# Kernel tuning notes

Hardware: AMD Instinct MI355X
Metric: run time of the kernel (lower is better)

The kernel has to match this reference:

```python
import jax, jax.numpy as jnp
import numpy as np
import math

B, L, D = 2, 2048, 1024
H = 16
DH = D // H  # 64
XPOS_SCALE_BASE = 512.0
THETA = 10000.0


def setup_inputs() -> dict:
    key = jax.random.key(0)
    ks = jax.random.split(key, 9)
    s = 0.02  # keep logits in a sane range like trained weights
    return {
        "x": jax.random.normal(ks[0], (B, L, D), dtype=jnp.float32),
        "Wq": jax.random.normal(ks[1], (D, D), dtype=jnp.float32) * s,
        "bq": jax.random.normal(ks[2], (D,), dtype=jnp.float32) * s,
        "Wk": jax.random.normal(ks[3], (D, D), dtype=jnp.float32) * s,
        "bk": jax.random.normal(ks[4], (D,), dtype=jnp.float32) * s,
        "Wv": jax.random.normal(ks[5], (D, D), dtype=jnp.float32) * s,
        "bv": jax.random.normal(ks[6], (D,), dtype=jnp.float32) * s,
        "Wo": jax.random.normal(ks[7], (D, D), dtype=jnp.float32) * s,
        "bo": jax.random.normal(ks[8], (D,), dtype=jnp.float32) * s,
    }


def _rotate_half(t):
    # pairwise interleaved rotation, as in rotary_embedding_torch
    t1 = t[..., 0::2]
    t2 = t[..., 1::2]
    return jnp.stack([-t2, t1], axis=-1).reshape(t.shape)


def _xpos_rotate(q, k):
    # q, k: [B, H, L, DH]; xPos rotary embedding (use_xpos=True)
    seq = q.shape[2]
    half = jnp.arange(0, DH, 2, dtype=jnp.float32)
    inv_freq = 1.0 / (THETA ** (half / DH))            # [DH/2]
    t = jnp.arange(seq, dtype=jnp.float32)             # [L]
    freqs = t[:, None] * inv_freq[None, :]             # [L, DH/2]
    freqs = jnp.repeat(freqs, 2, axis=-1)              # [L, DH] interleaved
    # xPos length-extrapolatable scale
    scale_vec = (half + 0.4 * DH) / (1.4 * DH)         # [DH/2]
    power = (t - seq // 2) / XPOS_SCALE_BASE           # [L]
    scale = scale_vec[None, :] ** power[:, None]       # [L, DH/2]
    scale = jnp.repeat(scale, 2, axis=-1)              # [L, DH]
    cos = jnp.cos(freqs)
    sin = jnp.sin(freqs)
    q_out = q * (cos * scale) + _rotate_half(q) * (sin * scale)
    k_out = k * (cos / scale) + _rotate_half(k) * (sin / scale)
    return q_out, k_out


def reference(x, Wq, bq, Wk, bk, Wv, bv, Wo, bo):
    b, l, d = x.shape
    # projections; note source swaps names: v_mat <- k-proj, k_mat <- v-proj
    q = (x @ Wq.T + bq).reshape(b, l, H, DH).transpose(0, 2, 1, 3)  # [b,h,l,dh]
    v = (x @ Wk.T + bk).reshape(b, l, H, DH).transpose(0, 2, 1, 3)
    k = (x @ Wv.T + bv).reshape(b, l, H, DH).transpose(0, 2, 1, 3)
    q, k = _xpos_rotate(q, k)
    # source divides by sqrt(Dh * num_heads) == sqrt(dim)
    scores = jnp.einsum("bhqd,bhkd->bhqk", q, k) / math.sqrt(d)
    weights = jax.nn.softmax(scores, axis=-1)
    inter = jnp.einsum("bhqk,bhkd->bhqd", weights, v)
    inter = inter.transpose(0, 2, 1, 3).reshape(b, l, d)
    return inter @ Wo.T + bo
```

## Files before the change

kernel.cpp:

```cpp
#include <hip/hip_runtime.h>
#include <math.h>

#define NB 2
#define NL 2048
#define ND 1024
#define NH 16
#define NDH 64
#define NBL 4096

typedef __attribute__((ext_vector_type(4)))  float f32x4;
typedef __attribute__((ext_vector_type(16))) float f32x16;
typedef __attribute__((ext_vector_type(8)))  short s16x8;
typedef __attribute__((ext_vector_type(4)))  short s16x4;

#define LOG2E 1.44269504088896f

__device__ __forceinline__ float fexp2(float x){
#if __has_builtin(__builtin_amdgcn_exp2f)
  return __builtin_amdgcn_exp2f(x);
#else
  return exp2f(x);
#endif
}

__device__ __forceinline__ unsigned short f2bf(float f){
  unsigned int u = __float_as_uint(f);
  u += 0x7FFF + ((u >> 16) & 1);
  return (unsigned short)(u >> 16);
}

__device__ __forceinline__ unsigned int pk2bf(float lo, float hi){
  return __builtin_amdgcn_perm(__float_as_uint(hi) + 0x8000u,
                               __float_as_uint(lo) + 0x8000u, 0x07060302u);
}

__global__ void cvt_all(const float* __restrict__ x,
                        const float* __restrict__ wq, const float* __restrict__ wk,
                        const float* __restrict__ wv, const float* __restrict__ wo,
                        unsigned short* __restrict__ xb,
                        unsigned short* __restrict__ wqb, unsigned short* __restrict__ wkb,
                        unsigned short* __restrict__ wvb, unsigned short* __restrict__ wob){
  int i = blockIdx.x * blockDim.x + threadIdx.x;
  const float* s; unsigned short* d; int off;
  if (i < (1<<20)) { s = x; d = xb; off = i; }
  else {
    int j = i - (1<<20); int w = j >> 18; off = j & ((1<<18)-1);
    s = (w==0)?wq:(w==1)?wk:(w==2)?wv:wo;
    d = (w==0)?wqb:(w==1)?wkb:(w==2)?wvb:wob;
  }
  float4 f = reinterpret_cast<const float4*>(s)[off];
  ushort4 r; r.x=f2bf(f.x); r.y=f2bf(f.y); r.z=f2bf(f.z); r.w=f2bf(f.w);
  reinterpret_cast<ushort4*>(d)[off] = r;
}

__global__ void rope_tables(float2* __restrict__ qtab, float2* __restrict__ ktab){
  int t = blockIdx.x * blockDim.x + threadIdx.x;
  int l = t >> 5, i = t & 31;
  float half = 2.0f * (float)i;
  float inv_freq = 1.0f / powf(10000.0f, half / 64.0f);
  float fr = (float)l * inv_freq;
  float sv = (half + 0.4f * 64.0f) / (1.4f * 64.0f);
  float pw = ((float)l - 1024.0f) / 512.0f;
  float sc = powf(sv, pw);
  float cs = cosf(fr), sn = sinf(fr);
  qtab[t] = make_float2(cs * sc, sn * sc);
  ktab[t] = make_float2(cs / sc, sn / sc);
}

__device__ __forceinline__ void gemm_core128(
    const unsigned short* __restrict__ A, const unsigned short* __restrict__ W,
    int row0, int col0,
    unsigned short (&As)[128][32], unsigned short (&Bs)[128][32],
    f32x4 (&acc)[4][4])
{
  const int tid  = threadIdx.x;
  const int wave = tid >> 6, lane = tid & 63;
  const int m16  = lane & 15, quad = lane >> 4;
  const int mrow = (wave & 1) * 64, ncol = (wave >> 1) * 64;
  const int rA   = lane >> 2, cA = (lane & 3) * 8;

  for (int k0 = 0; k0 < ND; k0 += 32){
    __syncthreads();
#pragma unroll
    for (int i2 = 0; i2 < 2; i2++){
      const int c = wave * 2 + i2;
      const unsigned short* ga = A + (size_t)(row0 + c*16 + rA) * ND + k0 + cA;
      const unsigned short* gb = W + (size_t)(col0 + c*16 + rA) * ND + k0 + cA;
      __builtin_amdgcn_global_load_lds((const __attribute__((address_space(1))) void*)ga,
                                       (__attribute__((address_space(3))) void*)&As[c*16][0], 16, 0, 0);
      __builtin_amdgcn_global_load_lds((const __attribute__((address_space(1))) void*)gb,
                                       (__attribute__((address_space(3))) void*)&Bs[c*16][0], 16, 0, 0);
    }
    __syncthreads();
    s16x8 af[4], bf[4];
#pragma unroll
    for (int mt = 0; mt < 4; mt++) af[mt] = *reinterpret_cast<const s16x8*>(&As[mrow + mt*16 + m16][quad*8]);
#pragma unroll
    for (int nt = 0; nt < 4; nt++) bf[nt] = *reinterpret_cast<const s16x8*>(&Bs[ncol + nt*16 + m16][quad*8]);
#pragma unroll
    for (int mt = 0; mt < 4; mt++)
#pragma unroll
      for (int nt = 0; nt < 4; nt++)
        acc[mt][nt] = __builtin_amdgcn_mfma_f32_16x16x32_bf16(af[mt], bf[nt], acc[mt][nt], 0, 0, 0);
  }
}

__global__ __launch_bounds__(256) void gemm_qkv(
    const unsigned short* __restrict__ A,
    const unsigned short* __restrict__ Wq, const float* __restrict__ bq,
    const unsigned short* __restrict__ Wk, const float* __restrict__ bk,
    const unsigned short* __restrict__ Wv, const float* __restrict__ bv,
    unsigned short* __restrict__ qb, unsigned short* __restrict__ kb,
    unsigned short* __restrict__ vtb,
    const float2* __restrict__ qtab, const float2* __restrict__ ktab)
{
  __shared__ unsigned short As[128][32];
  __shared__ unsigned short Bs[128][32];
  __shared__ unsigned short T[128][72];

  const int mode = blockIdx.z;
  const unsigned short* W = (mode==0) ? Wq : (mode==1) ? Wk : Wv;
  const float* bias       = (mode==0) ? bq : (mode==1) ? bk : bv;

  const int row0 = blockIdx.x * 128, col0 = blockIdx.y * 128;
  f32x4 acc[4][4] = {};
  gemm_core128(A, W, row0, col0, As, Bs, acc);

  const int tid  = threadIdx.x;
  const int wave = tid >> 6, lane = tid & 63;
  const int m16  = lane & 15, quad = lane >> 4;
  const int mrow = (wave & 1) * 64, ncol = (wave >> 1) * 64;

  if (mode == 2){
    const int b = row0 >> 11, l0 = row0 & (NL - 1);
#pragma unroll
    for (int h2 = 0; h2 < 2; h2++){
      __syncthreads();
      if ((wave >> 1) == h2){
#pragma unroll
        for (int mt = 0; mt < 4; mt++)
#pragma unroll
          for (int nt = 0; nt < 4; nt++)
#pragma unroll
            for (int r = 0; r < 4; r++){
              int lrow = mrow + mt*16 + quad*4 + r;
              int dh   = nt*16 + m16;
              T[lrow][dh] = f2bf(acc[mt][nt][r] + bias[col0 + h2*64 + dh]);
            }
      }
      __syncthreads();
      const int bh = b * NH + (col0 >> 6) + h2;
#pragma unroll
      for (int j4 = 0; j4 < 4; j4++){
        int c = tid * 4 + j4;
        int d = c >> 4, seg = (c & 15) * 8;
        unsigned short tmp[8];
#pragma unroll
        for (int jj = 0; jj < 8; jj++) tmp[jj] = T[seg + jj][d];
        *reinterpret_cast<uint4*>(vtb + (size_t)(bh * NDH + d) * NL + l0 + seg) =
            *reinterpret_cast<uint4*>(tmp);
      }
    }
  } else {
    const float qscale = (mode == 0) ? (0.03125f * LOG2E) : 1.0f;
    const float2* tab  = (mode == 0) ? qtab : ktab;
    unsigned short* dst = (mode == 0) ? qb : kb;
#pragma unroll
    for (int mt = 0; mt < 4; mt++)
#pragma unroll
      for (int nt = 0; nt < 4; nt++)
#pragma unroll
        for (int r = 0; r < 4; r++){
          int grow = row0 + mrow + mt*16 + quad*4 + r;
          int gcol = col0 + ncol + nt*16 + m16;
          float v = acc[mt][nt][r] + bias[gcol];
          int b = grow >> 11, l = grow & (NL - 1);
          int h = gcol >> 6, dh = gcol & 63;
          float pv = __shfl_xor(v, 1);
          float2 t = tab[l*32 + (dh >> 1)];
          float rh = (dh & 1) ? pv : -pv;
          float ov = (v * t.x + rh * t.y) * qscale;
          dst[(((size_t)(b * NH + h)) * NL + l) * NDH + dh] = f2bf(ov);
        }
  }
}

__global__ __launch_bounds__(256) void gemm_o(
    const unsigned short* __restrict__ A, const unsigned short* __restrict__ W,
    const float* __restrict__ bias, float* __restrict__ out)
{
  __shared__ unsigned short As[128][32];
  __shared__ unsigned short Bs[64][32];
  const int tid  = threadIdx.x;
  const int wave = tid >> 6, lane = tid & 63;
  const int m16  = lane & 15, quad = lane >> 4;
  const int mrow = (wave & 1) * 64, ncol = (wave >> 1) * 32;
  const int rA   = lane >> 2, cA = (lane & 3) * 8;
  const int row0 = blockIdx.x * 128, col0 = blockIdx.y * 64;

  f32x4 acc[4][2] = {};

  for (int k0 = 0; k0 < ND; k0 += 32){
    __syncthreads();
#pragma unroll
    for (int i3 = 0; i3 < 3; i3++){
      const int c = wave * 3 + i3;
      const unsigned short* g; unsigned short* l;
      if (c < 8){ g = A + (size_t)(row0 + c*16 + rA) * ND + k0 + cA;      l = &As[c*16][0]; }
      else      { g = W + (size_t)(col0 + (c-8)*16 + rA) * ND + k0 + cA;  l = &Bs[(c-8)*16][0]; }
      __builtin_amdgcn_global_load_lds((const __attribute__((address_space(1))) void*)g,
                                       (__attribute__((address_space(3))) void*)l, 16, 0, 0);
    }
    __syncthreads();
    s16x8 af[4], bf[2];
#pragma unroll
    for (int mt = 0; mt < 4; mt++) af[mt] = *reinterpret_cast<const s16x8*>(&As[mrow + mt*16 + m16][quad*8]);
#pragma unroll
    for (int nt = 0; nt < 2; nt++) bf[nt] = *reinterpret_cast<const s16x8*>(&Bs[ncol + nt*16 + m16][quad*8]);
#pragma unroll
    for (int mt = 0; mt < 4; mt++)
#pragma unroll
      for (int nt = 0; nt < 2; nt++)
        acc[mt][nt] = __builtin_amdgcn_mfma_f32_16x16x32_bf16(af[mt], bf[nt], acc[mt][nt], 0, 0, 0);
  }

#pragma unroll
  for (int mt = 0; mt < 4; mt++)
#pragma unroll
    for (int nt = 0; nt < 2; nt++)
#pragma unroll
      for (int r = 0; r < 4; r++){
        int grow = row0 + mrow + mt*16 + quad*4 + r;
        int gcol = col0 + ncol + nt*16 + m16;
        out[(size_t)grow * ND + gcol] = acc[mt][nt][r] + bias[gcol];
      }
}

__global__ __launch_bounds__(256, 1) void attn_kernel(
    const unsigned short* __restrict__ qb,
    const unsigned short* __restrict__ kb,
    const unsigned short* __restrict__ vtb,
    unsigned short* __restrict__ ob)
{
  __shared__ unsigned short smem[256 * 72];
  const int tid  = threadIdx.x;
  const int wave = tid >> 6, lane = tid & 63;
  const int l31  = lane & 31, g = lane >> 5;
  const int bh   = blockIdx.y;
  const int q0   = blockIdx.x * 256;
  const unsigned short* Q  = qb  + (size_t)bh * NL * NDH;
  const unsigned short* K  = kb  + (size_t)bh * NL * NDH;
  const unsigned short* Vt = vtb + (size_t)bh * NDH * NL;

  s16x8 qf[2][4];
#pragma unroll
  for (int q2 = 0; q2 < 2; q2++)
#pragma unroll
    for (int s = 0; s < 4; s++)
      qf[q2][s] = *reinterpret_cast<const s16x8*>(
          Q + (size_t)(q0 + wave*64 + q2*32 + l31) * NDH + s*16 + g*8);

  const int r0 = tid >> 3,          c0 = tid & 7;
  const int r1 = (tid + 256) >> 3,  c1 = tid & 7;
  const int so0 = r0*64 + ((c0 ^ (r0 & 7)) * 8);
  const int so1 = r1*64 + ((c1 ^ (r1 & 7)) * 8);

  uint4 kreg0 = *reinterpret_cast<const uint4*>(K  + (size_t)r0 * NDH + c0*8);
  uint4 kreg1 = *reinterpret_cast<const uint4*>(K  + (size_t)r1 * NDH + c1*8);
  uint4 vreg0 = *reinterpret_cast<const uint4*>(Vt + (size_t)r0 * NL  + c0*8);
  uint4 vreg1 = *reinterpret_cast<const uint4*>(Vt + (size_t)r1 * NL  + c1*8);
  *reinterpret_cast<uint4*>(&smem[so0])         = kreg0;
  *reinterpret_cast<uint4*>(&smem[so1])         = kreg1;
  *reinterpret_cast<uint4*>(&smem[8192 + so0])  = vreg0;
  *reinterpret_cast<uint4*>(&smem[8192 + so1])  = vreg1;
  kreg0 = *reinterpret_cast<const uint4*>(K  + (size_t)(64 + r0) * NDH + c0*8);
  kreg1 = *reinterpret_cast<const uint4*>(K  + (size_t)(64 + r1) * NDH + c1*8);
  vreg0 = *reinterpret_cast<const uint4*>(Vt + (size_t)r0 * NL + 64 + c0*8);
  vreg1 = *reinterpret_cast<const uint4*>(Vt + (size_t)r1 * NL + 64 + c1*8);
  __syncthreads();

  float ls[2] = {0.f, 0.f};
  f32x16 ot[2][2] = {};
  const int key7 = l31 & 7;

  for (int kt = 0; kt < 32; kt++){
    const int cur = (kt & 1) * 4096;
    const int nxt = 4096 - cur;
    if (kt < 31){
      *reinterpret_cast<uint4*>(&smem[nxt + so0])        = kreg0;
      *reinterpret_cast<uint4*>(&smem[nxt + so1])        = kreg1;
      *reinterpret_cast<uint4*>(&smem[8192 + nxt + so0]) = vreg0;
      *reinterpret_cast<uint4*>(&smem[8192 + nxt + so1]) = vreg1;
    }
    if (kt < 30){
      const int k0n = (kt + 2) * 64;
      kreg0 = *reinterpret_cast<const uint4*>(K  + (size_t)(k0n + r0) * NDH + c0*8);
      kreg1 = *reinterpret_cast<const uint4*>(K  + (size_t)(k0n + r1) * NDH + c1*8);
      vreg0 = *reinterpret_cast<const uint4*>(Vt + (size_t)r0 * NL + k0n + c0*8);
      vreg1 = *reinterpret_cast<const uint4*>(Vt + (size_t)r1 * NL + k0n + c1*8);
    }

    const unsigned short* Kb = &smem[cur];
    const unsigned short* Vb = &smem[8192 + cur];

    unsigned int pe[2][2][8];
#pragma unroll
    for (int t = 0; t < 2; t++){
      f32x16 st0 = {}, st1 = {};
#pragma unroll
      for (int s = 0; s < 4; s++){
        const int cg = (2*s + g) ^ key7;
        s16x8 kf = *reinterpret_cast<const s16x8*>(&Kb[(t*32 + l31)*64 + cg*8]);
        st0 = __builtin_amdgcn_mfma_f32_32x32x16_bf16(kf, qf[0][s], st0, 0, 0, 0);
        st1 = __builtin_amdgcn_mfma_f32_32x32x16_bf16(kf, qf[1][s], st1, 0, 0, 0);
      }
#pragma unroll
      for (int i = 0; i < 8; i++){
        float a0 = fexp2(st0[2*i]), a1 = fexp2(st0[2*i+1]);
        ls[0] += a0 + a1;
        pe[0][t][i] = pk2bf(a0, a1);
        float b0 = fexp2(st1[2*i]), b1 = fexp2(st1[2*i+1]);
        ls[1] += b0 + b1;
        pe[1][t][i] = pk2bf(b0, b1);
      }
    }

#pragma unroll
    for (int mt = 0; mt < 2; mt++){
      const int dh = mt*32 + l31;
#pragma unroll
      for (int s = 0; s < 8; s++){
        const int cg = s ^ (dh & 7);
        s16x4 vf = *reinterpret_cast<const s16x4*>(&Vb[dh*64 + cg*8 + g*4]);
        uint2 pb0; pb0.x = pe[0][s>>2][2*(s&3)]; pb0.y = pe[0][s>>2][2*(s&3)+1];
        ot[mt][0] = __builtin_amdgcn_mfma_f32_32x32x8bf16_1k(
            vf, *reinterpret_cast<s16x4*>(&pb0), ot[mt][0], 0, 0, 0);
        uint2 pb1; pb1.x = pe[1][s>>2][2*(s&3)]; pb1.y = pe[1][s>>2][2*(s&3)+1];
        ot[mt][1] = __builtin_amdgcn_mfma_f32_32x32x8bf16_1k(
            vf, *reinterpret_cast<s16x4*>(&pb1), ot[mt][1], 0, 0, 0);
      }
    }
    __syncthreads();
  }

  float linv[2];
#pragma unroll
  for (int q2 = 0; q2 < 2; q2++){
    float t = ls[q2] + __shfl_xor(ls[q2], 32);
    linv[q2] = 1.0f / t;
  }

#pragma unroll
  for (int mt = 0; mt < 2; mt++)
#pragma unroll
    for (int q2 = 0; q2 < 2; q2++)
#pragma unroll
      for (int s = 0; s < 4; s++){
        float o0 = ot[mt][q2][4*s    ] * linv[q2];
        float o1 = ot[mt][q2][4*s + 1] * linv[q2];
        float o2 = ot[mt][q2][4*s + 2] * linv[q2];
        float o3 = ot[mt][q2][4*s + 3] * linv[q2];
        uint2 pk; pk.x = pk2bf(o0, o1); pk.y = pk2bf(o2, o3);
        *reinterpret_cast<uint2*>(&smem[(wave*64 + q2*32 + l31)*72 + mt*32 + s*8 + g*4]) = pk;
      }
  __syncthreads();

  const int bb = bh >> 4, h = bh & 15;
#pragma unroll
  for (int j = 0; j < 8; j++){
    int idx = j*256 + tid;
    int row = idx >> 3, cg2 = (idx & 7) * 8;
    *reinterpret_cast<uint4*>(ob + ((size_t)(bb*NL + q0 + row)) * ND + h*NDH + cg2) =
        *reinterpret_cast<const uint4*>(&smem[row*72 + cg2]);
  }
}

extern "C" void kernel_launch(void* const* d_in, const int* in_sizes, int n_in,
                              void* d_out, int out_size, void* d_ws, size_t ws_size,
                              hipStream_t stream)
{
  (void)in_sizes; (void)n_in; (void)out_size; (void)ws_size;
  const float* x  = (const float*)d_in[0];
  const float* Wq = (const float*)d_in[1];
  const float* bq = (const float*)d_in[2];
  const float* Wk = (const float*)d_in[3];
  const float* bk = (const float*)d_in[4];
  const float* Wv = (const float*)d_in[5];
  const float* bv = (const float*)d_in[6];
  const float* Wo = (const float*)d_in[7];
  const float* bo = (const float*)d_in[8];
  float* out = (float*)d_out;

  char* p = (char*)d_ws;
  unsigned short* xb   = (unsigned short*)p; p += (size_t)NBL*ND*2;
  unsigned short* wqb  = (unsigned short*)p; p += (size_t)ND*ND*2;
  unsigned short* wkb  = (unsigned short*)p; p += (size_t)ND*ND*2;
  unsigned short* wvb  = (unsigned short*)p; p += (size_t)ND*ND*2;
  unsigned short* wob  = (unsigned short*)p; p += (size_t)ND*ND*2;
  unsigned short* qbuf = (unsigned short*)p; p += (size_t)NBL*ND*2;
  unsigned short* kbuf = (unsigned short*)p; p += (size_t)NBL*ND*2;
  unsigned short* vtb  = (unsigned short*)p; p += (size_t)NBL*ND*2;
  unsigned short* ibuf = (unsigned short*)p; p += (size_t)NBL*ND*2;
  float2* qtab = (float2*)p; p += (size_t)NL*32*8;
  float2* ktab = (float2*)p; p += (size_t)NL*32*8;

  hipLaunchKernelGGL(cvt_all, dim3(8192), dim3(256), 0, stream,
                     x, Wq, Wk, Wv, Wo, xb, wqb, wkb, wvb, wob);
  hipLaunchKernelGGL(rope_tables, dim3(NL*32/256), dim3(256), 0, stream, qtab, ktab);

  hipLaunchKernelGGL(gemm_qkv, dim3(NBL/128, ND/128, 3), dim3(256), 0, stream,
                     xb, wqb, bq, wvb, bv, wkb, bk, qbuf, kbuf, vtb, qtab, ktab);

  hipLaunchKernelGGL(attn_kernel, dim3(NL/256, NB*NH), dim3(256), 0, stream,
                     qbuf, kbuf, vtb, ibuf);

  hipLaunchKernelGGL(gemm_o, dim3(NBL/128, ND/64), dim3(256), 0, stream, ibuf, wob, bo, out);
}
```

Baseline: 208.9 us.

## Split attention keys across wave pairs, stage QK epilogue via LDS, fuse rope tables

The attention kernel now handles 128 queries per block and splits the 2048 keys between two wave pairs. The partial outputs and row sums are merged through LDS, and the grid doubles to 512 blocks with occupancy 2. The QKV GEMM epilogue for Q and K stages results in shared memory so global stores are coalesced, and it gains a launch-bounds occupancy hint. The rope table computation is folded into the conversion kernel to drop one launch. The key split adds an LDS reduction, an extra sync, and a bf16 rounding of the partial sums.

```diff
diff --git a/kernel.cpp b/kernel.cpp
--- a/kernel.cpp
+++ b/kernel.cpp
@@ -39,73 +39,36 @@
                         const float* __restrict__ wv, const float* __restrict__ wo,
                         unsigned short* __restrict__ xb,
                         unsigned short* __restrict__ wqb, unsigned short* __restrict__ wkb,
-                        unsigned short* __restrict__ wvb, unsigned short* __restrict__ wob){
+                        unsigned short* __restrict__ wvb, unsigned short* __restrict__ wob,
+                        float2* __restrict__ qtab, float2* __restrict__ ktab){
   int i = blockIdx.x * blockDim.x + threadIdx.x;
-  const float* s; unsigned short* d; int off;
-  if (i < (1<<20)) { s = x; d = xb; off = i; }
-  else {
-    int j = i - (1<<20); int w = j >> 18; off = j & ((1<<18)-1);
-    s = (w==0)?wq:(w==1)?wk:(w==2)?wv:wo;
-    d = (w==0)?wqb:(w==1)?wkb:(w==2)?wvb:wob;
-  }
-  float4 f = reinterpret_cast<const float4*>(s)[off];
-  ushort4 r; r.x=f2bf(f.x); r.y=f2bf(f.y); r.z=f2bf(f.z); r.w=f2bf(f.w);
-  reinterpret_cast<ushort4*>(d)[off] = r;
-}
-
-__global__ void rope_tables(float2* __restrict__ qtab, float2* __restrict__ ktab){
-  int t = blockIdx.x * blockDim.x + threadIdx.x;
-  int l = t >> 5, i = t & 31;
-  float half = 2.0f * (float)i;
-  float inv_freq = 1.0f / powf(10000.0f, half / 64.0f);
-  float fr = (float)l * inv_freq;
-  float sv = (half + 0.4f * 64.0f) / (1.4f * 64.0f);
-  float pw = ((float)l - 1024.0f) / 512.0f;
-  float sc = powf(sv, pw);
-  float cs = cosf(fr), sn = sinf(fr);
-  qtab[t] = make_float2(cs * sc, sn * sc);
-  ktab[t] = make_float2(cs / sc, sn / sc);
-}
-
-__device__ __forceinline__ void gemm_core128(
-    const unsigned short* __restrict__ A, const unsigned short* __restrict__ W,
-    int row0, int col0,
-    unsigned short (&As)[128][32], unsigned short (&Bs)[128][32],
-    f32x4 (&acc)[4][4])
-{
-  const int tid  = threadIdx.x;
-  const int wave = tid >> 6, lane = tid & 63;
-  const int m16  = lane & 15, quad = lane >> 4;
-  const int mrow = (wave & 1) * 64, ncol = (wave >> 1) * 64;
-  const int rA   = lane >> 2, cA = (lane & 3) * 8;
-
-  for (int k0 = 0; k0 < ND; k0 += 32){
-    __syncthreads();
-#pragma unroll
-    for (int i2 = 0; i2 < 2; i2++){
-      const int c = wave * 2 + i2;
-      const unsigned short* ga = A + (size_t)(row0 + c*16 + rA) * ND + k0 + cA;
-      const unsigned short* gb = W + (size_t)(col0 + c*16 + rA) * ND + k0 + cA;
-      __builtin_amdgcn_global_load_lds((const __attribute__((address_space(1))) void*)ga,
-                                       (__attribute__((address_space(3))) void*)&As[c*16][0], 16, 0, 0);
-      __builtin_amdgcn_global_load_lds((const __attribute__((address_space(1))) void*)gb,
-                                       (__attribute__((address_space(3))) void*)&Bs[c*16][0], 16, 0, 0);
-    }
-    __syncthreads();
-    s16x8 af[4], bf[4];
-#pragma unroll
-    for (int mt = 0; mt < 4; mt++) af[mt] = *reinterpret_cast<const s16x8*>(&As[mrow + mt*16 + m16][quad*8]);
-#pragma unroll
-    for (int nt = 0; nt < 4; nt++) bf[nt] = *reinterpret_cast<const s16x8*>(&Bs[ncol + nt*16 + m16][quad*8]);
-#pragma unroll
-    for (int mt = 0; mt < 4; mt++)
-#pragma unroll
-      for (int nt = 0; nt < 4; nt++)
-        acc[mt][nt] = __builtin_amdgcn_mfma_f32_16x16x32_bf16(af[mt], bf[nt], acc[mt][nt], 0, 0, 0);
-  }
-}
-
-__global__ __launch_bounds__(256) void gemm_qkv(
+  if (i < (1<<21)){
+    const float* s; unsigned short* d; int off;
+    if (i < (1<<20)) { s = x; d = xb; off = i; }
+    else {
+      int j = i - (1<<20); int w = j >> 18; off = j & ((1<<18)-1);
+      s = (w==0)?wq:(w==1)?wk:(w==2)?wv:wo;
+      d = (w==0)?wqb:(w==1)?wkb:(w==2)?wvb:wob;
+    }
+    float4 f = reinterpret_cast<const float4*>(s)[off];
+    ushort4 r; r.x=f2bf(f.x); r.y=f2bf(f.y); r.z=f2bf(f.z); r.w=f2bf(f.w);
+    reinterpret_cast<ushort4*>(d)[off] = r;
+  } else {
+    int t = i - (1<<21);
+    int l = t >> 5, k = t & 31;
+    float half = 2.0f * (float)k;
+    float inv_freq = 1.0f / powf(10000.0f, half / 64.0f);
+    float fr = (float)l * inv_freq;
+    float sv = (half + 0.4f * 64.0f) / (1.4f * 64.0f);
+    float pw = ((float)l - 1024.0f) / 512.0f;
+    float sc = powf(sv, pw);
+    float cs = cosf(fr), sn = sinf(fr);
+    qtab[t] = make_float2(cs * sc, sn * sc);
+    ktab[t] = make_float2(cs / sc, sn / sc);
+  }
+}
+
+__global__ __launch_bounds__(256, 3) void gemm_qkv(
     const unsigned short* __restrict__ A,
     const unsigned short* __restrict__ Wq, const float* __restrict__ bq,
     const unsigned short* __restrict__ Wk, const float* __restrict__ bk,
@@ -114,29 +77,55 @@
     unsigned short* __restrict__ vtb,
     const float2* __restrict__ qtab, const float2* __restrict__ ktab)
 {
-  __shared__ unsigned short As[128][32];
-  __shared__ unsigned short Bs[128][32];
-  __shared__ unsigned short T[128][72];
+  __shared__ unsigned short smem[9216];
 
   const int mode = blockIdx.z;
   const unsigned short* W = (mode==0) ? Wq : (mode==1) ? Wk : Wv;
   const float* bias       = (mode==0) ? bq : (mode==1) ? bk : bv;
-
-  const int row0 = blockIdx.x * 128, col0 = blockIdx.y * 128;
-  f32x4 acc[4][4] = {};
-  gemm_core128(A, W, row0, col0, As, Bs, acc);
 
   const int tid  = threadIdx.x;
   const int wave = tid >> 6, lane = tid & 63;
   const int m16  = lane & 15, quad = lane >> 4;
   const int mrow = (wave & 1) * 64, ncol = (wave >> 1) * 64;
-
-  if (mode == 2){
-    const int b = row0 >> 11, l0 = row0 & (NL - 1);
-#pragma unroll
-    for (int h2 = 0; h2 < 2; h2++){
-      __syncthreads();
-      if ((wave >> 1) == h2){
+  const int rA   = lane >> 2, cA = (lane & 3) * 8;
+  const int row0 = blockIdx.x * 128, col0 = blockIdx.y * 128;
+
+  f32x4 acc[4][4] = {};
+
+  for (int k0 = 0; k0 < ND; k0 += 32){
+    __syncthreads();
+#pragma unroll
+    for (int i2 = 0; i2 < 2; i2++){
+      const int c = wave * 2 + i2;
+      const unsigned short* ga = A + (size_t)(row0 + c*16 + rA) * ND + k0 + cA;
+      const unsigned short* gb = W + (size_t)(col0 + c*16 + rA) * ND + k0 + cA;
+      __builtin_amdgcn_global_load_lds((const __attribute__((address_space(1))) void*)ga,
+                                       (__attribute__((address_space(3))) void*)&smem[c*512], 16, 0, 0);
+      __builtin_amdgcn_global_load_lds((const __attribute__((address_space(1))) void*)gb,
+                                       (__attribute__((address_space(3))) void*)&smem[4096 + c*512], 16, 0, 0);
+    }
+    __syncthreads();
+    s16x8 af[4], bf[4];
+#pragma unroll
+    for (int mt = 0; mt < 4; mt++)
+      af[mt] = *reinterpret_cast<const s16x8*>(&smem[(mrow + mt*16 + m16)*32 + quad*8]);
+#pragma unroll
+    for (int nt = 0; nt < 4; nt++)
+      bf[nt] = *reinterpret_cast<const s16x8*>(&smem[4096 + (ncol + nt*16 + m16)*32 + quad*8]);
+#pragma unroll
+    for (int mt = 0; mt < 4; mt++)
+#pragma unroll
+      for (int nt = 0; nt < 4; nt++)
+        acc[mt][nt] = __builtin_amdgcn_mfma_f32_16x16x32_bf16(af[mt], bf[nt], acc[mt][nt], 0, 0, 0);
+  }
+  __syncthreads();
+
+  const int b  = row0 >> 11, l0 = row0 & (NL - 1);
+
+#pragma unroll
+  for (int h2 = 0; h2 < 2; h2++){
+    if ((wave >> 1) == h2){
+      if (mode == 2){
 #pragma unroll
         for (int mt = 0; mt < 4; mt++)
 #pragma unroll
@@ -145,43 +134,57 @@
             for (int r = 0; r < 4; r++){
               int lrow = mrow + mt*16 + quad*4 + r;
               int dh   = nt*16 + m16;
-              T[lrow][dh] = f2bf(acc[mt][nt][r] + bias[col0 + h2*64 + dh]);
+              smem[lrow*72 + dh] = f2bf(acc[mt][nt][r] + bias[col0 + h2*64 + dh]);
             }
-      }
-      __syncthreads();
-      const int bh = b * NH + (col0 >> 6) + h2;
+      } else {
+        const float qscale = (mode == 0) ? (0.03125f * LOG2E) : 1.0f;
+        const float2* tab  = (mode == 0) ? qtab : ktab;
+#pragma unroll
+        for (int mt = 0; mt < 4; mt++)
+#pragma unroll
+          for (int nt = 0; nt < 4; nt++)
+#pragma unroll
+            for (int r = 0; r < 4; r++){
+              int lrow = mrow + mt*16 + quad*4 + r;
+              int dh   = nt*16 + m16;
+              float v  = acc[mt][nt][r] + bias[col0 + h2*64 + dh];
+              float pv = __shfl_xor(v, 1);
+              float2 t = tab[(l0 + lrow)*32 + (dh >> 1)];
+              float rh = (dh & 1) ? pv : -pv;
+              smem[lrow*72 + dh] = f2bf((v * t.x + rh * t.y) * qscale);
+            }
+      }
+    }
+    __syncthreads();
+
+    const int bh = b * NH + (col0 >> 6) + h2;
+    if (mode == 2){
 #pragma unroll
       for (int j4 = 0; j4 < 4; j4++){
         int c = tid * 4 + j4;
         int d = c >> 4, seg = (c & 15) * 8;
         unsigned short tmp[8];
 #pragma unroll
-        for (int jj = 0; jj < 8; jj++) tmp[jj] = T[seg + jj][d];
+        for (int jj = 0; jj < 8; jj++) tmp[jj] = smem[(seg + jj)*72 + d];
         *reinterpret_cast<uint4*>(vtb + (size_t)(bh * NDH + d) * NL + l0 + seg) =
             *reinterpret_cast<uint4*>(tmp);
       }
-    }
-  } else {
-    const float qscale = (mode == 0) ? (0.03125f * LOG2E) : 1.0f;
-    const float2* tab  = (mode == 0) ? qtab : ktab;
-    unsigned short* dst = (mode == 0) ? qb : kb;
-#pragma unroll
-    for (int mt = 0; mt < 4; mt++)
-#pragma unroll
-      for (int nt = 0; nt < 4; nt++)
-#pragma unroll
-        for (int r = 0; r < 4; r++){
-          int grow = row0 + mrow + mt*16 + quad*4 + r;
-          int gcol = col0 + ncol + nt*16 + m16;
-          float v = acc[mt][nt][r] + bias[gcol];
-          int b = grow >> 11, l = grow & (NL - 1);
-          int h = gcol >> 6, dh = gcol & 63;
-          float pv = __shfl_xor(v, 1);
-          float2 t = tab[l*32 + (dh >> 1)];
-          float rh = (dh & 1) ? pv : -pv;
-          float ov = (v * t.x + rh * t.y) * qscale;
-          dst[(((size_t)(b * NH + h)) * NL + l) * NDH + dh] = f2bf(ov);
-        }
+    } else {
+      unsigned short* dst = ((mode == 0) ? qb : kb) + ((size_t)bh * NL + l0) * NDH;
+#pragma unroll
+      for (int j = 0; j < 2; j++){
+        int idx = j*256 + tid;
+        (void)idx;
+      }
+#pragma unroll
+      for (int j = 0; j < 4; j++){
+        int idx = j*256 + tid;
+        int row = idx >> 3, cg = (idx & 7) * 8;
+        *reinterpret_cast<uint4*>(dst + row*NDH + cg) =
+            *reinterpret_cast<const uint4*>(&smem[row*72 + cg]);
+      }
+    }
+    __syncthreads();
   }
 }
 
@@ -236,18 +239,20 @@
       }
 }
 
-__global__ __launch_bounds__(256, 1) void attn_kernel(
+__global__ __launch_bounds__(256, 2) void attn_kernel(
     const unsigned short* __restrict__ qb,
     const unsigned short* __restrict__ kb,
     const unsigned short* __restrict__ vtb,
     unsigned short* __restrict__ ob)
 {
-  __shared__ unsigned short smem[256 * 72];
+  __shared__ unsigned short smem[32768];
   const int tid  = threadIdx.x;
   const int wave = tid >> 6, lane = tid & 63;
   const int l31  = lane & 31, g = lane >> 5;
+  const int half = wave >> 1, w2 = wave & 1;
   const int bh   = blockIdx.y;
-  const int q0   = blockIdx.x * 256;
+  const int q0   = blockIdx.x * 128;
+  const int khalf = half * (NL / 2);
   const unsigned short* Q  = qb  + (size_t)bh * NL * NDH;
   const unsigned short* K  = kb  + (size_t)bh * NL * NDH;
   const unsigned short* Vt = vtb + (size_t)bh * NDH * NL;
@@ -258,52 +263,58 @@
 #pragma unroll
     for (int s = 0; s < 4; s++)
       qf[q2][s] = *reinterpret_cast<const s16x8*>(
-          Q + (size_t)(q0 + wave*64 + q2*32 + l31) * NDH + s*16 + g*8);
-
-  const int r0 = tid >> 3,          c0 = tid & 7;
-  const int r1 = (tid + 256) >> 3,  c1 = tid & 7;
-  const int so0 = r0*64 + ((c0 ^ (r0 & 7)) * 8);
-  const int so1 = r1*64 + ((c1 ^ (r1 & 7)) * 8);
-
-  uint4 kreg0 = *reinterpret_cast<const uint4*>(K  + (size_t)r0 * NDH + c0*8);
-  uint4 kreg1 = *reinterpret_cast<const uint4*>(K  + (size_t)r1 * NDH + c1*8);
-  uint4 vreg0 = *reinterpret_cast<const uint4*>(Vt + (size_t)r0 * NL  + c0*8);
-  uint4 vreg1 = *reinterpret_cast<const uint4*>(Vt + (size_t)r1 * NL  + c1*8);
-  *reinterpret_cast<uint4*>(&smem[so0])         = kreg0;
-  *reinterpret_cast<uint4*>(&smem[so1])         = kreg1;
-  *reinterpret_cast<uint4*>(&smem[8192 + so0])  = vreg0;
-  *reinterpret_cast<uint4*>(&smem[8192 + so1])  = vreg1;
-  kreg0 = *reinterpret_cast<const uint4*>(K  + (size_t)(64 + r0) * NDH + c0*8);
-  kreg1 = *reinterpret_cast<const uint4*>(K  + (size_t)(64 + r1) * NDH + c1*8);
-  vreg0 = *reinterpret_cast<const uint4*>(Vt + (size_t)r0 * NL + 64 + c0*8);
-  vreg1 = *reinterpret_cast<const uint4*>(Vt + (size_t)r1 * NL + 64 + c1*8);
+          Q + (size_t)(q0 + w2*64 + q2*32 + l31) * NDH + s*16 + g*8);
+
+  const int ht = tid & 127;
+  const int rr = ht >> 3, cc = ht & 7;
+  const int HB = half * 16384;
+  const int so0 = rr*64 + ((cc ^ (rr & 7)) * 8);
+
+  uint4 kr[4], vr[4];
+#pragma unroll
+  for (int p = 0; p < 4; p++){
+    kr[p] = *reinterpret_cast<const uint4*>(K  + (size_t)(khalf + rr + 16*p) * NDH + cc*8);
+    vr[p] = *reinterpret_cast<const uint4*>(Vt + (size_t)(rr + 16*p) * NL + khalf + cc*8);
+  }
+#pragma unroll
+  for (int p = 0; p < 4; p++){
+    *reinterpret_cast<uint4*>(&smem[HB + so0 + p*1024])        = kr[p];
+    *reinterpret_cast<uint4*>(&smem[HB + 8192 + so0 + p*1024]) = vr[p];
+  }
+#pragma unroll
+  for (int p = 0; p < 4; p++){
+    kr[p] = *reinterpret_cast<const uint4*>(K  + (size_t)(khalf + 64 + rr + 16*p) * NDH + cc*8);
+    vr[p] = *reinterpret_cast<const uint4*>(Vt + (size_t)(rr + 16*p) * NL + khalf + 64 + cc*8);
+  }
   __syncthreads();
 
   float ls[2] = {0.f, 0.f};
   f32x16 ot[2][2] = {};
   const int key7 = l31 & 7;
 
-  for (int kt = 0; kt < 32; kt++){
-    const int cur = (kt & 1) * 4096;
-    const int nxt = 4096 - cur;
-    if (kt < 31){
-      *reinterpret_cast<uint4*>(&smem[nxt + so0])        = kreg0;
-      *reinterpret_cast<uint4*>(&smem[nxt + so1])        = kreg1;
-      *reinterpret_cast<uint4*>(&smem[8192 + nxt + so0]) = vreg0;
-      *reinterpret_cast<uint4*>(&smem[8192 + nxt + so1]) = vreg1;
-    }
-    if (kt < 30){
-      const int k0n = (kt + 2) * 64;
-      kreg0 = *reinterpret_cast<const uint4*>(K  + (size_t)(k0n + r0) * NDH + c0*8);
-      kreg1 = *reinterpret_cast<const uint4*>(K  + (size_t)(k0n + r1) * NDH + c1*8);
-      vreg0 = *reinterpret_cast<const uint4*>(Vt + (size_t)r0 * NL + k0n + c0*8);
-      vreg1 = *reinterpret_cast<const uint4*>(Vt + (size_t)r1 * NL + k0n + c1*8);
+  for (int kt = 0; kt < 16; kt++){
+    const int cur = HB + (kt & 1) * 4096;
+    const int nxt = HB + (((kt & 1) ^ 1)) * 4096;
+    if (kt < 15){
+#pragma unroll
+      for (int p = 0; p < 4; p++){
+        *reinterpret_cast<uint4*>(&smem[nxt + so0 + p*1024])        = kr[p];
+        *reinterpret_cast<uint4*>(&smem[nxt + 8192 + so0 + p*1024]) = vr[p];
+      }
+    }
+    if (kt < 14){
+      const int k0n = khalf + (kt + 2) * 64;
+#pragma unroll
+      for (int p = 0; p < 4; p++){
+        kr[p] = *reinterpret_cast<const uint4*>(K  + (size_t)(k0n + rr + 16*p) * NDH + cc*8);
+        vr[p] = *reinterpret_cast<const uint4*>(Vt + (size_t)(rr + 16*p) * NL + k0n + cc*8);
+      }
     }
 
     const unsigned short* Kb = &smem[cur];
-    const unsigned short* Vb = &smem[8192 + cur];
-
-    unsigned int pe[2][2][8];
+    const unsigned short* Vb = &smem[cur + 8192];
+
+    uint2 pmat[2][8];
 #pragma unroll
     for (int t = 0; t < 2; t++){
       f32x16 st0 = {}, st1 = {};
@@ -315,13 +326,17 @@
         st1 = __builtin_amdgcn_mfma_f32_32x32x16_bf16(kf, qf[1][s], st1, 0, 0, 0);
       }
 #pragma unroll
-      for (int i = 0; i < 8; i++){
-        float a0 = fexp2(st0[2*i]), a1 = fexp2(st0[2*i+1]);
-        ls[0] += a0 + a1;
-        pe[0][t][i] = pk2bf(a0, a1);
-        float b0 = fexp2(st1[2*i]), b1 = fexp2(st1[2*i+1]);
-        ls[1] += b0 + b1;
-        pe[1][t][i] = pk2bf(b0, b1);
+      for (int j = 0; j < 4; j++){
+        float a0 = fexp2(st0[4*j]),   a1 = fexp2(st0[4*j+1]);
+        float a2 = fexp2(st0[4*j+2]), a3 = fexp2(st0[4*j+3]);
+        ls[0] += (a0 + a1) + (a2 + a3);
+        pmat[0][t*4+j].x = pk2bf(a0, a1);
+        pmat[0][t*4+j].y = pk2bf(a2, a3);
+        float b0 = fexp2(st1[4*j]),   b1 = fexp2(st1[4*j+1]);
+        float b2 = fexp2(st1[4*j+2]), b3 = fexp2(st1[4*j+3]);
+        ls[1] += (b0 + b1) + (b2 + b3);
+        pmat[1][t*4+j].x = pk2bf(b0, b1);
+        pmat[1][t*4+j].y = pk2bf(b2, b3);
       }
     }
 
@@ -332,42 +347,65 @@
       for (int s = 0; s < 8; s++){
         const int cg = s ^ (dh & 7);
         s16x4 vf = *reinterpret_cast<const s16x4*>(&Vb[dh*64 + cg*8 + g*4]);
-        uint2 pb0; pb0.x = pe[0][s>>2][2*(s&3)]; pb0.y = pe[0][s>>2][2*(s&3)+1];
         ot[mt][0] = __builtin_amdgcn_mfma_f32_32x32x8bf16_1k(
-            vf, *reinterpret_cast<s16x4*>(&pb0), ot[mt][0], 0, 0, 0);
-        uint2 pb1; pb1.x = pe[1][s>>2][2*(s&3)]; pb1.y = pe[1][s>>2][2*(s&3)+1];
+            vf, *reinterpret_cast<s16x4*>(&pmat[0][s]), ot[mt][0], 0, 0, 0);
         ot[mt][1] = __builtin_amdgcn_mfma_f32_32x32x8bf16_1k(
-            vf, *reinterpret_cast<s16x4*>(&pb1), ot[mt][1], 0, 0, 0);
-      }
-    }
-    __syncthreads();
-  }
-
-  float linv[2];
-#pragma unroll
-  for (int q2 = 0; q2 < 2; q2++){
-    float t = ls[q2] + __shfl_xor(ls[q2], 32);
-    linv[q2] = 1.0f / t;
-  }
-
-#pragma unroll
-  for (int mt = 0; mt < 2; mt++)
+            vf, *reinterpret_cast<s16x4*>(&pmat[1][s]), ot[mt][1], 0, 0, 0);
+      }
+    }
+    __syncthreads();
+  }
+
+  float* lsb = reinterpret_cast<float*>(&smem[20480]);
+  if (half == 0){
 #pragma unroll
     for (int q2 = 0; q2 < 2; q2++)
-#pragma unroll
-      for (int s = 0; s < 4; s++){
-        float o0 = ot[mt][q2][4*s    ] * linv[q2];
-        float o1 = ot[mt][q2][4*s + 1] * linv[q2];
-        float o2 = ot[mt][q2][4*s + 2] * linv[q2];
-        float o3 = ot[mt][q2][4*s + 3] * linv[q2];
-        uint2 pk; pk.x = pk2bf(o0, o1); pk.y = pk2bf(o2, o3);
-        *reinterpret_cast<uint2*>(&smem[(wave*64 + q2*32 + l31)*72 + mt*32 + s*8 + g*4]) = pk;
-      }
+      lsb[((w2*2 + q2)*2 + g)*32 + l31] = ls[q2];
+#pragma unroll
+    for (int mt = 0; mt < 2; mt++)
+#pragma unroll
+      for (int q2 = 0; q2 < 2; q2++)
+#pragma unroll
+        for (int s = 0; s < 4; s++){
+          uint2 pk;
+          pk.x = pk2bf(ot[mt][q2][4*s],     ot[mt][q2][4*s + 1]);
+          pk.y = pk2bf(ot[mt][q2][4*s + 2], ot[mt][q2][4*s + 3]);
+          *reinterpret_cast<uint2*>(&smem[(w2*64 + q2*32 + l31)*72 + mt*32 + s*8 + g*4]) = pk;
+        }
+  }
   __syncthreads();
+  if (half == 1){
+    float linv[2];
+#pragma unroll
+    for (int q2 = 0; q2 < 2; q2++){
+      float t = ls[q2] + __shfl_xor(ls[q2], 32)
+              + lsb[((w2*2 + q2)*2 + 0)*32 + l31]
+              + lsb[((w2*2 + q2)*2 + 1)*32 + l31];
+      linv[q2] = 1.0f / t;
+    }
+#pragma unroll
+    for (int mt = 0; mt < 2; mt++)
+#pragma unroll
+      for (int q2 = 0; q2 < 2; q2++)
+#pragma unroll
+        for (int s = 0; s < 4; s++){
+          unsigned short* ad = &smem[(w2*64 + q2*32 + l31)*72 + mt*32 + s*8 + g*4];
+          uint2 u = *reinterpret_cast<const uint2*>(ad);
+          float p0 = __uint_as_float(u.x << 16)          + ot[mt][q2][4*s];
+          float p1 = __uint_as_float(u.x & 0xFFFF0000u)  + ot[mt][q2][4*s + 1];
+          float p2 = __uint_as_float(u.y << 16)          + ot[mt][q2][4*s + 2];
+          float p3 = __uint_as_float(u.y & 0xFFFF0000u)  + ot[mt][q2][4*s + 3];
+          uint2 pk;
+          pk.x = pk2bf(p0 * linv[q2], p1 * linv[q2]);
+          pk.y = pk2bf(p2 * linv[q2], p3 * linv[q2]);
+          *reinterpret_cast<uint2*>(ad) = pk;
+        }
+  }
+  __syncthreads();
 
   const int bb = bh >> 4, h = bh & 15;
 #pragma unroll
-  for (int j = 0; j < 8; j++){
+  for (int j = 0; j < 4; j++){
     int idx = j*256 + tid;
     int row = idx >> 3, cg2 = (idx & 7) * 8;
     *reinterpret_cast<uint4*>(ob + ((size_t)(bb*NL + q0 + row)) * ND + h*NDH + cg2) =
@@ -404,14 +442,13 @@
   float2* qtab = (float2*)p; p += (size_t)NL*32*8;
   float2* ktab = (float2*)p; p += (size_t)NL*32*8;
 
-  hipLaunchKernelGGL(cvt_all, dim3(8192), dim3(256), 0, stream,
-                     x, Wq, Wk, Wv, Wo, xb, wqb, wkb, wvb, wob);
-  hipLaunchKernelGGL(rope_tables, dim3(NL*32/256), dim3(256), 0, stream, qtab, ktab);
+  hipLaunchKernelGGL(cvt_all, dim3(8448), dim3(256), 0, stream,
+                     x, Wq, Wk, Wv, Wo, xb, wqb, wkb, wvb, wob, qtab, ktab);
 
   hipLaunchKernelGGL(gemm_qkv, dim3(NBL/128, ND/128, 3), dim3(256), 0, stream,
                      xb, wqb, bq, wvb, bv, wkb, bk, qbuf, kbuf, vtb, qtab, ktab);
 
-  hipLaunchKernelGGL(attn_kernel, dim3(NL/256, NB*NH), dim3(256), 0, stream,
+  hipLaunchKernelGGL(attn_kernel, dim3(NL/128, NB*NH), dim3(256), 0, stream,
                      qbuf, kbuf, vtb, ibuf);
 
   hipLaunchKernelGGL(gemm_o, dim3(NBL/128, ND/64), dim3(256), 0, stream, ibuf, wob, bo, out);
```

Measured after the change: 217.1 us. +3.9%, slower.
